# Kernel optimization log

Hardware: AMD Instinct MI355X
Metric: run time of the kernel (lower is better)

Reference implementation:

```python
import jax, jax.numpy as jnp
import numpy as np

IN_FEATURES = 256
OUT_FEATURES = 256


def setup_inputs() -> dict:
    key = jax.random.key(0)
    kx, kw, ks, kb = jax.random.split(key, 4)
    x = jax.random.normal(kx, (131072, IN_FEATURES), dtype=jnp.float32)
    # Xavier-uniform init for the latent fp weight [out, in]
    limit = float(np.sqrt(6.0 / (IN_FEATURES + OUT_FEATURES)))
    W = jax.random.uniform(kw, (OUT_FEATURES, IN_FEATURES), dtype=jnp.float32,
                           minval=-limit, maxval=limit)
    # scale initialized to ones in the module; perturb slightly to make it non-trivial
    scale = jnp.ones((OUT_FEATURES,), dtype=jnp.float32) + 0.01 * jax.random.normal(ks, (OUT_FEATURES,), dtype=jnp.float32)
    bias = 0.01 * jax.random.normal(kb, (OUT_FEATURES,), dtype=jnp.float32)
    return {"x": x, "W": W, "scale": scale, "bias": bias}


def reference(x, W, scale, bias):
    # STE binarization: forward value is sign(W), gradient passes through to W
    binary_w = W + jax.lax.stop_gradient(jnp.sign(W) - W)          # [out, in]
    scaled_w = binary_w * scale[:, None]                           # per-output-channel rescale
    # F.linear(x, scaled_w, bias) = x @ scaled_w.T + bias
    return jnp.einsum('bi,oi->bo', x, scaled_w) + bias
```

## Files before the change

### kernel.cpp

```cpp
#include <hip/hip_runtime.h>
#include <hip/hip_bf16.h>


typedef __bf16 bf16_t;
typedef __attribute__((ext_vector_type(8))) __bf16 bf16x8;
typedef __attribute__((ext_vector_type(4))) float f32x4;

#define MROWS 131072
#define NDIM 256
#define KDIM 256
#define TROWS 16
#define NT (MROWS / TROWS)
#define TILES 8
#define GRID (NT / TILES)

__global__ __launch_bounds__(256) void prep_w_kernel(const float* __restrict__ W,
                                                     bf16_t* __restrict__ wb) {
    int idx = blockIdx.x * 256 + threadIdx.x;
    float w = W[idx];
    wb[idx] = (bf16_t)((w > 0.0f) ? 1.0f : ((w < 0.0f) ? -1.0f : 0.0f));
}

__device__ inline bf16x8 cvt8(f32x4 lo, f32x4 hi) {
    bf16x8 r;
    r[0] = (bf16_t)lo.x; r[1] = (bf16_t)lo.y; r[2] = (bf16_t)lo.z; r[3] = (bf16_t)lo.w;
    r[4] = (bf16_t)hi.x; r[5] = (bf16_t)hi.y; r[6] = (bf16_t)hi.z; r[7] = (bf16_t)hi.w;
    return r;
}

__global__ __launch_bounds__(256, 2) void bin_gemm_kernel(
        const float* __restrict__ x,
        const bf16_t* __restrict__ wb,
        const float* __restrict__ scale,
        const float* __restrict__ bias,
        float* __restrict__ out) {
    const int tid  = threadIdx.x;
    const int lane = tid & 63;
    const int wave = tid >> 6;
    const int lrow = lane & 15;
    const int lk   = lane >> 4;
    const int cb   = wave * 64;

    bf16x8 breg[4][8];
    #pragma unroll
    for (int ni = 0; ni < 4; ++ni) {
        const bf16_t* pb = wb + (size_t)(cb + ni * 16 + lrow) * KDIM + lk * 8;
        #pragma unroll
        for (int ks = 0; ks < 8; ++ks)
            breg[ni][ks] = *reinterpret_cast<const bf16x8*>(pb + ks * 32);
    }
    float sc[4], bi[4];
    #pragma unroll
    for (int ni = 0; ni < 4; ++ni) {
        sc[ni] = scale[cb + ni * 16 + lrow];
        bi[ni] = bias[cb + ni * 16 + lrow];
    }

    const int t0 = blockIdx.x * TILES;
    for (int ti = 0; ti < TILES; ++ti) {
        const int t = t0 + ti;
        const float* px = x + ((size_t)t * TROWS + lrow) * KDIM + lk * 8;

        f32x4 xlo[8], xhi[8];
        #pragma unroll
        for (int ks = 0; ks < 8; ++ks) {
            xlo[ks] = *reinterpret_cast<const f32x4*>(px + ks * 32);
            xhi[ks] = *reinterpret_cast<const f32x4*>(px + ks * 32 + 4);
        }
        __builtin_amdgcn_sched_barrier(0);

        bf16x8 a[8];
        #pragma unroll
        for (int ks = 0; ks < 8; ++ks) a[ks] = cvt8(xlo[ks], xhi[ks]);

        f32x4 acc[4] = {};
        #pragma unroll
        for (int ks = 0; ks < 8; ++ks)
            #pragma unroll
            for (int ni = 0; ni < 4; ++ni)
                acc[ni] = __builtin_amdgcn_mfma_f32_16x16x32_bf16(
                              a[ks], breg[ni][ks], acc[ni], 0, 0, 0);

        float* po = out + ((size_t)t * TROWS + lk * 4) * NDIM;
        #pragma unroll
        for (int ni = 0; ni < 4; ++ni) {
            int col = cb + ni * 16 + lrow;
            #pragma unroll
            for (int r = 0; r < 4; ++r)
                po[(size_t)r * NDIM + col] = acc[ni][r] * sc[ni] + bi[ni];
        }
    }
}

extern "C" void kernel_launch(void* const* d_in, const int* in_sizes, int n_in,
                              void* d_out, int out_size, void* d_ws, size_t ws_size,
                              hipStream_t stream) {
    const float* x     = (const float*)d_in[0];
    const float* W     = (const float*)d_in[1];
    const float* scale = (const float*)d_in[2];
    const float* bias  = (const float*)d_in[3];
    float*       out   = (float*)d_out;
    bf16_t*      wb    = (bf16_t*)d_ws;

    prep_w_kernel<<<NDIM * KDIM / 256, 256, 0, stream>>>(W, wb);
    bin_gemm_kernel<<<GRID, 256, 0, stream>>>(x, wb, scale, bias, out);
}
```

Measured before the change: 268.4 us.

## Stage x tiles through double-buffered LDS with async global_load_lds prefetch

Before this change, all four waves loaded the same 16x256 x tile from global memory directly into registers. Now the block cooperatively copies each tile once into LDS using global_load_lds with an XOR swizzle, and double-buffers so the next tile's load overlaps the current tile's MFMA work. The goal is to cut redundant global loads and hide memory latency. In exchange it adds 32KB of LDS per block, which may limit occupancy, plus two barriers per tile.

```diff
diff --git a/kernel.cpp b/kernel.cpp
--- a/kernel.cpp
+++ b/kernel.cpp
@@ -10,9 +10,8 @@
 #define NDIM 256
 #define KDIM 256
 #define TROWS 16
-#define NT (MROWS / TROWS)
 #define TILES 8
-#define GRID (NT / TILES)
+#define GRID (MROWS / (TROWS * TILES))
 
 __global__ __launch_bounds__(256) void prep_w_kernel(const float* __restrict__ W,
                                                      bf16_t* __restrict__ wb) {
@@ -28,12 +27,28 @@
     return r;
 }
 
+__device__ inline void stage_tile(char* dst, const float* xt, int tid) {
+    const char* src = (const char*)xt;
+    #pragma unroll
+    for (int p = 0; p < 4; ++p) {
+        int s = p * 256 + tid;
+        int r = s >> 6;
+        int c = s & 63;
+        __builtin_amdgcn_global_load_lds(
+            (const __attribute__((address_space(1))) void*)(src + r * 1024 + ((c ^ (r & 7)) * 16)),
+            (__attribute__((address_space(3))) void*)(dst + p * 4096 + (tid & 192) * 16),
+            16, 0, 0);
+    }
+}
+
 __global__ __launch_bounds__(256, 2) void bin_gemm_kernel(
         const float* __restrict__ x,
         const bf16_t* __restrict__ wb,
         const float* __restrict__ scale,
         const float* __restrict__ bias,
         float* __restrict__ out) {
+    __shared__ __align__(16) char xlds[2][16384];
+
     const int tid  = threadIdx.x;
     const int lane = tid & 63;
     const int wave = tid >> 6;
@@ -57,31 +72,33 @@
     }
 
     const int t0 = blockIdx.x * TILES;
+    stage_tile(xlds[0], x + (size_t)t0 * TROWS * KDIM, tid);
+
+    const int swz = lrow & 7;
     for (int ti = 0; ti < TILES; ++ti) {
-        const int t = t0 + ti;
-        const float* px = x + ((size_t)t * TROWS + lrow) * KDIM + lk * 8;
+        __builtin_amdgcn_s_barrier();
+        if (ti + 1 < TILES)
+            stage_tile(xlds[(ti + 1) & 1], x + (size_t)(t0 + ti + 1) * TROWS * KDIM, tid);
+        if (ti + 1 < TILES) asm volatile("s_waitcnt vmcnt(4)" ::: "memory");
+        else                asm volatile("s_waitcnt vmcnt(0)" ::: "memory");
+        __builtin_amdgcn_sched_barrier(0);
+        __builtin_amdgcn_s_barrier();
 
-        f32x4 xlo[8], xhi[8];
+        const char* cur = xlds[ti & 1] + lrow * 1024;
+        f32x4 acc[4] = {};
         #pragma unroll
         for (int ks = 0; ks < 8; ++ks) {
-            xlo[ks] = *reinterpret_cast<const f32x4*>(px + ks * 32);
-            xhi[ks] = *reinterpret_cast<const f32x4*>(px + ks * 32 + 4);
-        }
-        __builtin_amdgcn_sched_barrier(0);
-
-        bf16x8 a[8];
-        #pragma unroll
-        for (int ks = 0; ks < 8; ++ks) a[ks] = cvt8(xlo[ks], xhi[ks]);
-
-        f32x4 acc[4] = {};
-        #pragma unroll
-        for (int ks = 0; ks < 8; ++ks)
+            int c0 = ks * 8 + lk * 2;
+            f32x4 lo = *reinterpret_cast<const f32x4*>(cur + ((c0 ^ swz) * 16));
+            f32x4 hi = *reinterpret_cast<const f32x4*>(cur + (((c0 + 1) ^ swz) * 16));
+            bf16x8 a = cvt8(lo, hi);
             #pragma unroll
             for (int ni = 0; ni < 4; ++ni)
                 acc[ni] = __builtin_amdgcn_mfma_f32_16x16x32_bf16(
-                              a[ks], breg[ni][ks], acc[ni], 0, 0, 0);
+                              a, breg[ni][ks], acc[ni], 0, 0, 0);
+        }
 
-        float* po = out + ((size_t)t * TROWS + lk * 4) * NDIM;
+        float* po = out + ((size_t)(t0 + ti) * TROWS + lk * 4) * NDIM;
         #pragma unroll
         for (int ni = 0; ni < 4; ++ni) {
             int col = cb + ni * 16 + lrow;
```

Measured after the change: 245.6 us. -8.5%, faster.
